# Optimization experiments

Measured on AMD Instinct MI355X. Metric: run time of the kernel, lower is better.

The kernel has to match this reference:

```python
import jax, jax.numpy as jnp
import numpy as np

B, N, D = 2, 4096, 1024
DS = 1024           # state_dim (defaults to embed_dim)
H = 4096            # mlp hidden = int(embed_dim * 4.0)
EPS = 1e-5


def _layernorm(x, w, b):
    mu = jnp.mean(x, axis=-1, keepdims=True)
    var = jnp.mean((x - mu) ** 2, axis=-1, keepdims=True)
    return (x - mu) * jax.lax.rsqrt(var + EPS) * w + b


def _selective_scan(deltaA, deltaB_u):
    # deltaA: (B, N, 1), deltaB_u: (B, N, DS). Recurrence h_i = dA_i * h + dBu_i.
    def step(h, inp):
        dA, dBu = inp           # (B,1), (B,DS)
        h = dA * h + dBu
        return h, h
    h0 = jnp.zeros((deltaB_u.shape[0], deltaB_u.shape[2]), deltaB_u.dtype)
    _, ys = jax.lax.scan(step, h0,
                         (jnp.swapaxes(deltaA, 0, 1), jnp.swapaxes(deltaB_u, 0, 1)))
    return jnp.swapaxes(ys, 0, 1)   # (B, N, DS)


def _forward(x, norm1_w, norm1_b, gate_w, gate_b, state_w, state_b,
             out_w, out_b, norm2_w, norm2_b, mlp_w1, mlp_b1, mlp_w2, mlp_b2):
    xn = _layernorm(x, norm1_w, norm1_b)
    g = xn @ gate_w + gate_b                       # (B,N,2D)
    gate, gate_gate = jnp.split(g, 2, axis=-1)
    gate = jax.nn.silu(gate)
    gate_gate = jax.nn.silu(gate_gate)
    u = (xn * gate) @ state_w + state_b            # (B,N,DS)
    Bm = gate_gate @ state_w + state_b             # (B,N,DS)
    # A = -ones(DS) -> delta*A = -delta broadcast over DS; keep (B,N,1)
    delta = jax.nn.softplus(jnp.mean(xn @ state_w + state_b, axis=-1, keepdims=True))
    deltaA = jnp.exp(-delta)                       # (B,N,1)
    deltaB_u = delta * Bm * u                      # (B,N,DS)
    # C = ones -> y_i = C_i * h_i = h_i
    y = _selective_scan(deltaA, deltaB_u)
    ssm_out = y @ out_w + out_b
    x = x + ssm_out
    x2 = _layernorm(x, norm2_w, norm2_b)
    mlp = jax.nn.gelu(x2 @ mlp_w1 + mlp_b1, approximate=False) @ mlp_w2 + mlp_b2
    return x + mlp


def setup_inputs() -> dict:
    key = jax.random.key(0)
    ks = jax.random.split(key, 12)
    s = 0.02
    p = lambda k, shape: jax.random.normal(k, shape, jnp.float32) * s
    return {
        "x": jax.random.normal(ks[0], (B, N, D), jnp.float32),
        "norm1_w": jnp.ones((D,), jnp.float32), "norm1_b": jnp.zeros((D,), jnp.float32),
        "gate_w": p(ks[1], (D, 2 * D)), "gate_b": p(ks[2], (2 * D,)),
        "state_w": p(ks[3], (D, DS)), "state_b": p(ks[4], (DS,)),
        "out_w": p(ks[5], (DS, D)), "out_b": p(ks[6], (D,)),
        "norm2_w": jnp.ones((D,), jnp.float32), "norm2_b": jnp.zeros((D,), jnp.float32),
        "mlp_w1": p(ks[7], (D, H)), "mlp_b1": p(ks[8], (H,)),
        "mlp_w2": p(ks[9], (H, D)), "mlp_b2": p(ks[10], (D,)),
    }


def reference(x, norm1_w, norm1_b, gate_w, gate_b, state_w, state_b,
              out_w, out_b, norm2_w, norm2_b, mlp_w1, mlp_b1, mlp_w2, mlp_b2):
    return _forward(x, norm1_w, norm1_b, gate_w, gate_b, state_w, state_b,
                    out_w, out_b, norm2_w, norm2_b, mlp_w1, mlp_b1, mlp_w2, mlp_b2)
```

## Files before the change

kernel.cpp:

```cpp
#include <hip/hip_runtime.h>
#include <hip/hip_bf16.h>
#include <math.h>

#define B_   2
#define N_   4096
#define D_   1024
#define DS_  1024
#define HID_ 4096
#define ROWS (B_ * N_)

#define CHK 128
#define TCH 32

typedef __attribute__((ext_vector_type(8))) short bf16x8;
typedef __attribute__((ext_vector_type(4))) float f32x4;

#define ASG __attribute__((address_space(1)))
#define AS3 __attribute__((address_space(3)))

__device__ __forceinline__ float bf2f(unsigned short u) {
  union { float f; unsigned int i; } v; v.i = ((unsigned int)u) << 16; return v.f;
}
__device__ __forceinline__ unsigned short f2bf(float f) {
  union { float f; unsigned int i; } v; v.f = f;
  unsigned int r = v.i + 0x7fffu + ((v.i >> 16) & 1u);
  return (unsigned short)(r >> 16);
}

__global__ void means_kernel(const float* __restrict__ W, const float* __restrict__ bvec,
                             float* __restrict__ swmean, float* __restrict__ sbmean) {
  __shared__ float sm[4];
  int bid = blockIdx.x, t = threadIdx.x;
  const float* src = (bid < D_) ? (W + (size_t)bid * DS_) : bvec;
  float s = 0.f;
  for (int j = t; j < DS_; j += 256) s += src[j];
  for (int o = 32; o; o >>= 1) s += __shfl_down(s, o);
  if ((t & 63) == 0) sm[t >> 6] = s;
  __syncthreads();
  if (t == 0) {
    float r = (sm[0] + sm[1] + sm[2] + sm[3]) * (1.f / DS_);
    if (bid < D_) swmean[bid] = r; else sbmean[0] = r;
  }
}

__global__ void transpose_all_kernel(const float* __restrict__ gw, const float* __restrict__ sw,
                                     const float* __restrict__ ow, const float* __restrict__ w1,
                                     const float* __restrict__ w2,
                                     unsigned short* __restrict__ gwT, unsigned short* __restrict__ swT,
                                     unsigned short* __restrict__ owT, unsigned short* __restrict__ w1T,
                                     unsigned short* __restrict__ w2T) {
  __shared__ float tile[32][33];
  int b = blockIdx.x;
  const float* W; unsigned short* WT; int K, N, t0;
  if (b < 2048)      { W = gw; WT = gwT; K = 1024; N = 2048; t0 = b; }
  else if (b < 3072) { W = sw; WT = swT; K = 1024; N = 1024; t0 = b - 2048; }
  else if (b < 4096) { W = ow; WT = owT; K = 1024; N = 1024; t0 = b - 3072; }
  else if (b < 8192) { W = w1; WT = w1T; K = 1024; N = 4096; t0 = b - 4096; }
  else               { W = w2; WT = w2T; K = 4096; N = 1024; t0 = b - 8192; }
  int ntx = N >> 5;
  int bn = (t0 % ntx) * 32, bk = (t0 / ntx) * 32;
  int tx = threadIdx.x & 31, ty = threadIdx.x >> 5;
  for (int i = ty; i < 32; i += 8)
    tile[i][tx] = W[(size_t)(bk + i) * N + bn + tx];
  __syncthreads();
  for (int i = ty; i < 32; i += 8)
    WT[(size_t)(bn + i) * K + bk + tx] = f2bf(tile[tx][i]);
}

template<bool WITH_DELTA>
__global__ void ln_kernel(const float* __restrict__ x, const float* __restrict__ w,
                          const float* __restrict__ bb, unsigned short* __restrict__ out_bf,
                          const float* __restrict__ swmean, const float* __restrict__ sbmean,
                          float* __restrict__ delta, float* __restrict__ ea) {
  __shared__ float sm[8];
  __shared__ float bc[2];
  int row = blockIdx.x, t = threadIdx.x;
  const float* xr = x + (size_t)row * D_;
  float4 xv = ((const float4*)xr)[t];
  float s  = xv.x + xv.y + xv.z + xv.w;
  float sq = xv.x * xv.x + xv.y * xv.y + xv.z * xv.z + xv.w * xv.w;
  for (int o = 32; o; o >>= 1) { s += __shfl_down(s, o); sq += __shfl_down(sq, o); }
  if ((t & 63) == 0) { sm[t >> 6] = s; sm[4 + (t >> 6)] = sq; }
  __syncthreads();
  if (t == 0) {
    float ts = sm[0] + sm[1] + sm[2] + sm[3];
    float tq = sm[4] + sm[5] + sm[6] + sm[7];
    float mu = ts * (1.f / D_);
    float var = tq * (1.f / D_) - mu * mu;
    bc[0] = mu; bc[1] = rsqrtf(var + 1e-5f);
  }
  __syncthreads();
  float mu = bc[0], rs = bc[1];
  float4 wv = ((const float4*)w)[t];
  float4 bv = ((const float4*)bb)[t];
  float n0 = (xv.x - mu) * rs * wv.x + bv.x;
  float n1 = (xv.y - mu) * rs * wv.y + bv.y;
  float n2 = (xv.z - mu) * rs * wv.z + bv.z;
  float n3 = (xv.w - mu) * rs * wv.w + bv.w;
  ushort4 o4; o4.x = f2bf(n0); o4.y = f2bf(n1); o4.z = f2bf(n2); o4.w = f2bf(n3);
  ((ushort4*)(out_bf + (size_t)row * D_))[t] = o4;
  if (WITH_DELTA) {
    float4 sw = ((const float4*)swmean)[t];
    float d = n0 * sw.x + n1 * sw.y + n2 * sw.z + n3 * sw.w;
    for (int o = 32; o; o >>= 1) d += __shfl_down(d, o);
    if ((t & 63) == 0) sm[t >> 6] = d;
    __syncthreads();
    if (t == 0) {
      float z = sm[0] + sm[1] + sm[2] + sm[3] + sbmean[0];
      float dl = (z > 15.f) ? z : log1pf(__expf(z));
      delta[row] = dl;
      ea[row] = __expf(-dl);
    }
  }
}


#define BARX { __builtin_amdgcn_s_barrier(); __builtin_amdgcn_sched_barrier(0); }

#define RD_A(TAU, H) { const char* ab_ = smem + ((((TAU)&1)*2+(H))<<14); \
  _Pragma("unroll") for (int mm_ = 0; mm_ < MB_H; ++mm_) \
  _Pragma("unroll") for (int ks_ = 0; ks_ < 2; ++ks_) { \
    int r_ = wr*(16*MB_H) + mm_*16 + l15; \
    int by_ = r_*128 + ks_*64 + kq16; by_ ^= ((by_>>7)&7)<<4; \
    af[mm_][ks_] = *(const bf16x8*)(ab_ + by_); } }

#define RD_B(TAU, H, DST) { const char* bb_ = smemB + ((((TAU)&1)*2+(H)))*SB; \
  _Pragma("unroll") for (int nn_ = 0; nn_ < NB_H; ++nn_) \
  _Pragma("unroll") for (int ks_ = 0; ks_ < 2; ++ks_) { \
    int r_ = wc*(16*NB_H) + nn_*16 + l15; \
    int by_ = r_*128 + ks_*64 + kq16; by_ ^= ((by_>>7)&7)<<4; \
    DST[nn_][ks_] = *(const bf16x8*)(bb_ + by_); } }

#define MFMAQ(QA, QB, BF) { __builtin_amdgcn_s_setprio(1); \
  _Pragma("unroll") for (int m_ = 0; m_ < MB_H; ++m_) \
  _Pragma("unroll") for (int n_ = 0; n_ < NB_H; ++n_) \
  _Pragma("unroll") for (int k_ = 0; k_ < 2; ++k_) \
    acc[(QA)*MB_H+m_][(QB)*NB_H+n_] = __builtin_amdgcn_mfma_f32_16x16x32_bf16( \
        af[m_][k_], BF[n_][k_], acc[(QA)*MB_H+m_][(QB)*NB_H+n_], 0, 0, 0); \
  __builtin_amdgcn_s_setprio(0); }

template<int BN, int EPI>
__global__ __launch_bounds__(512, 2) void gemm8p(
    const unsigned short* __restrict__ A1p, int lda1, int M1,
    const unsigned short* __restrict__ A2p, int lda2,
    const unsigned short* __restrict__ BT, const float* __restrict__ bias,
    void* __restrict__ Cout, const float* __restrict__ res,
    int N, int K, int nbx) {
  constexpr int WN   = (BN == 256) ? 4 : 2;
  constexpr int MB_H = (BN == 256) ? 4 : 2;
  constexpr int NB_H = 2;
  constexpr int MF   = 2 * MB_H;
  constexpr int LB   = BN / 128;
  constexpr int SB   = (BN / 2) * 64 * 2;
  __shared__ char smem[65536 + 4 * SB];
  char* smemB = smem + 65536;

  const int nwg = gridDim.x;
  int bid = blockIdx.x;
  int wg = (bid & 7) * (nwg >> 3) + (bid >> 3);
  const int bx = wg % nbx, by = wg / nbx;
  const int mbase = by * 256, nbase = bx * BN;

  const int tid = threadIdx.x;
  const int lane = tid & 63, wid = tid >> 6;
  const int wr = wid / WN, wc = wid % WN;
  const int l15 = lane & 15, kq16 = (lane >> 4) * 16;
  const int wvoff16 = wid << 10;

  const unsigned short* Ause; int ldaU;
  if (mbase < M1) { Ause = A1p + (size_t)mbase * lda1; ldaU = lda1; }
  else            { Ause = A2p + (size_t)(mbase - M1) * lda2; ldaU = lda2; }

  int L0 = tid * 16;        int b0 = L0 ^ (((L0 >> 7) & 7) << 4);
  int L1 = 8192 + tid * 16; int b1 = L1 ^ (((L1 >> 7) & 7) << 4);
  const unsigned short* pA0 = Ause + (size_t)(b0 >> 7) * ldaU + ((b0 & 127) >> 1);
  const unsigned short* pA1 = Ause + (size_t)(b1 >> 7) * ldaU + ((b1 & 127) >> 1);
  const unsigned short* pB0 = BT + (size_t)(nbase + (b0 >> 7)) * K + ((b0 & 127) >> 1);
  const unsigned short* pB1 = BT + (size_t)(nbase + (b1 >> 7)) * K + ((b1 & 127) >> 1);

  auto stageA = [&](int tau, int h, bool en) {
    if (!en) return;
    char* l0 = smem + (((tau & 1) * 2 + h) << 14) + wvoff16;
    const unsigned short* g0 = pA0 + (size_t)h * 128 * ldaU + tau * 64;
    const unsigned short* g1 = pA1 + (size_t)h * 128 * ldaU + tau * 64;
    __builtin_amdgcn_global_load_lds((const ASG void*)g0, (AS3 void*)l0, 16, 0, 0);
    __builtin_amdgcn_global_load_lds((const ASG void*)g1, (AS3 void*)(l0 + 8192), 16, 0, 0);
  };
  auto stageB = [&](int tau, int h, bool en) {
    if (!en) return;
    char* l0 = smemB + ((tau & 1) * 2 + h) * SB + wvoff16;
    const unsigned short* g0 = pB0 + (size_t)h * (BN / 2) * K + tau * 64;
    __builtin_amdgcn_global_load_lds((const ASG void*)g0, (AS3 void*)l0, 16, 0, 0);
    if constexpr (LB == 2) {
      const unsigned short* g1 = pB1 + (size_t)h * (BN / 2) * K + tau * 64;
      __builtin_amdgcn_global_load_lds((const ASG void*)g1, (AS3 void*)(l0 + 8192), 16, 0, 0);
    }
  };
  auto vm_steady = [&]() {
    if constexpr (BN == 256) { asm volatile("s_waitcnt vmcnt(6)" ::: "memory"); }
    else                     { asm volatile("s_waitcnt vmcnt(5)" ::: "memory"); }
  };

  f32x4 acc[MF][4];
#pragma unroll
  for (int m = 0; m < MF; ++m)
#pragma unroll
    for (int n = 0; n < 4; ++n) acc[m][n] = (f32x4){0.f, 0.f, 0.f, 0.f};
  bf16x8 af[MB_H][2], bq0[NB_H][2], bq1[NB_H][2];

  const int NT = K >> 6, NI = NT >> 1;

  stageA(0, 0, true); stageB(0, 0, true); stageA(0, 1, true); stageB(0, 1, true);
  stageA(1, 0, true); stageB(1, 0, true); stageA(1, 1, true);
  vm_steady();
  BARX;

#pragma unroll 1
  for (int i = 0; i < NI; ++i) {
    const int t0 = 2 * i;
    const bool st = (i < NI - 1);
    stageB(t0 + 1, 1, true); RD_A(t0, 0); RD_B(t0, 0, bq0);
    BARX; MFMAQ(0, 0, bq0); BARX;
    stageA(t0 + 2, 0, st); RD_B(t0, 1, bq1);
    BARX; MFMAQ(0, 1, bq1); BARX;
    stageB(t0 + 2, 0, st); RD_A(t0, 1);
    BARX; MFMAQ(1, 1, bq1); BARX;
    stageA(t0 + 2, 1, st);
    if (st) { vm_steady(); } else { asm volatile("s_waitcnt vmcnt(0)" ::: "memory"); }
    BARX; MFMAQ(1, 0, bq0); BARX;
    stageB(t0 + 2, 1, st); RD_A(t0 + 1, 0); RD_B(t0 + 1, 0, bq0);
    BARX; MFMAQ(0, 0, bq0); BARX;
    stageA(t0 + 3, 0, st); RD_B(t0 + 1, 1, bq1);
    BARX; MFMAQ(0, 1, bq1); BARX;
    stageB(t0 + 3, 0, st); RD_A(t0 + 1, 1);
    BARX; MFMAQ(1, 1, bq1); BARX;
    stageA(t0 + 3, 1, st);
    if (st) vm_steady();
    BARX; MFMAQ(1, 0, bq0); BARX;
  }

  const int r0 = (lane >> 4) * 4;
#pragma unroll
  for (int mb = 0; mb < MF; ++mb) {
    int row = mbase + wr * (16 * MB_H) + (mb % MB_H) * 16 + (mb / MB_H) * 128 + r0;
#pragma unroll
    for (int nb = 0; nb < 4; ++nb) {
      int col = nbase + wc * (16 * NB_H) + (nb % NB_H) * 16 + (nb / NB_H) * (BN / 2) + l15;
      float bc = bias[col];
#pragma unroll
      for (int r = 0; r < 4; ++r) {
        float v = acc[mb][nb][r] + bc;
        size_t off = (size_t)(row + r) * N + col;
        if (EPI == 1) {
          v = v / (1.f + __expf(-v));
          ((unsigned short*)Cout)[off] = f2bf(v);
        } else if (EPI == 2) {
          ((unsigned short*)Cout)[off] = f2bf(v);
        } else if (EPI == 3) {
          ((float*)Cout)[off] = v + res[off];
        } else if (EPI == 4) {
          float tt = v * (0.7978845608f + 0.0356774081f * v * v);
          v = v / (1.f + __expf(-2.f * tt));
          ((unsigned short*)Cout)[off] = f2bf(v);
        }
      }
    }
  }
}

__global__ void ew_xg_kernel(const unsigned short* __restrict__ xn,
                             const unsigned short* __restrict__ gs,
                             unsigned short* __restrict__ xg) {
  size_t i8 = ((size_t)blockIdx.x * 256 + threadIdx.x) * 8;
  size_t row = i8 >> 10, col = i8 & 1023;
  uint4 xv = *(const uint4*)(xn + i8);
  uint4 gv = *(const uint4*)(gs + row * 2048 + col);
  const unsigned short* xs = (const unsigned short*)&xv;
  const unsigned short* gg = (const unsigned short*)&gv;
  uint4 ov; unsigned short* o = (unsigned short*)&ov;
#pragma unroll
  for (int j = 0; j < 8; ++j) o[j] = f2bf(bf2f(xs[j]) * bf2f(gg[j]));
  *(uint4*)(xg + i8) = ov;
}

__global__ void scan_a_kernel(const unsigned short* __restrict__ u,
                              const unsigned short* __restrict__ bm,
                              const float* __restrict__ delta,
                              const float* __restrict__ ea,
                              float* __restrict__ hend, float* __restrict__ P) {
  int blk = blockIdx.x;
  int b = blk / CHK, c = blk % CHK;
  int ch = threadIdx.x;
  size_t base = ((size_t)(b * N_ + c * TCH)) * DS_ + ch;
  const float* dp = delta + b * N_ + c * TCH;
  const float* ep = ea + b * N_ + c * TCH;
  float h = 0.f, pa = 1.f;
#pragma unroll 4
  for (int t = 0; t < TCH; ++t) {
    float dl = dp[t], e = ep[t];
    float du = dl * bf2f(u[base + (size_t)t * DS_]) * bf2f(bm[base + (size_t)t * DS_]);
    h = e * h + du;
    pa *= e;
  }
  hend[(size_t)blk * DS_ + ch] = h;
  if (ch == 0) P[blk] = pa;
}

__global__ void scan_combine_kernel(const float* __restrict__ hend, const float* __restrict__ P,
                                    float* __restrict__ carryin) {
  int b = blockIdx.x, ch = threadIdx.x;
  float carry = 0.f;
  for (int c = 0; c < CHK; ++c) {
    size_t o = (size_t)(b * CHK + c) * DS_ + ch;
    carryin[o] = carry;
    carry = P[b * CHK + c] * carry + hend[o];
  }
}

__global__ void scan_b_kernel(const unsigned short* __restrict__ u,
                              const unsigned short* __restrict__ bm,
                              const float* __restrict__ delta,
                              const float* __restrict__ ea,
                              const float* __restrict__ carryin,
                              unsigned short* __restrict__ y) {
  int blk = blockIdx.x;
  int b = blk / CHK, c = blk % CHK;
  int ch = threadIdx.x;
  size_t base = ((size_t)(b * N_ + c * TCH)) * DS_ + ch;
  const float* dp = delta + b * N_ + c * TCH;
  const float* ep = ea + b * N_ + c * TCH;
  float h = carryin[(size_t)blk * DS_ + ch];
#pragma unroll 4
  for (int t = 0; t < TCH; ++t) {
    float dl = dp[t], e = ep[t];
    float du = dl * bf2f(u[base + (size_t)t * DS_]) * bf2f(bm[base + (size_t)t * DS_]);
    h = e * h + du;
    y[base + (size_t)t * DS_] = f2bf(h);
  }
}

extern "C" void kernel_launch(void* const* d_in, const int* in_sizes, int n_in,
                              void* d_out, int out_size, void* d_ws, size_t ws_size,
                              hipStream_t stream) {
  const float* x       = (const float*)d_in[0];
  const float* n1w     = (const float*)d_in[1];
  const float* n1b     = (const float*)d_in[2];
  const float* gate_w  = (const float*)d_in[3];
  const float* gate_b  = (const float*)d_in[4];
  const float* state_w = (const float*)d_in[5];
  const float* state_b = (const float*)d_in[6];
  const float* out_w   = (const float*)d_in[7];
  const float* out_b   = (const float*)d_in[8];
  const float* n2w     = (const float*)d_in[9];
  const float* n2b     = (const float*)d_in[10];
  const float* mlp_w1  = (const float*)d_in[11];
  const float* mlp_b1  = (const float*)d_in[12];
  const float* mlp_w2  = (const float*)d_in[13];
  const float* mlp_b2  = (const float*)d_in[14];
  float* outp = (float*)d_out;

  char* w = (char*)d_ws;
  size_t off = 0;
  auto alloc = [&](size_t bytes) { char* p = w + off; off += (bytes + 255) & ~(size_t)255; return p; };

  unsigned short* gate_wT  = (unsigned short*)alloc((size_t)2048 * 1024 * 2);
  unsigned short* state_wT = (unsigned short*)alloc((size_t)1024 * 1024 * 2);
  unsigned short* out_wT   = (unsigned short*)alloc((size_t)1024 * 1024 * 2);
  unsigned short* w1T      = (unsigned short*)alloc((size_t)4096 * 1024 * 2);
  unsigned short* w2T      = (unsigned short*)alloc((size_t)1024 * 4096 * 2);
  float* swmean  = (float*)alloc(D_ * 4);
  float* sbmean  = (float*)alloc(256);
  float* delta   = (float*)alloc((size_t)ROWS * 4);
  float* eadel   = (float*)alloc((size_t)ROWS * 4);
  float* hend    = (float*)alloc((size_t)B_ * CHK * DS_ * 4);
  float* carryin = (float*)alloc((size_t)B_ * CHK * DS_ * 4);
  float* P       = (float*)alloc((size_t)B_ * CHK * 4);
  unsigned short* xn = (unsigned short*)alloc((size_t)ROWS * D_ * 2);
  unsigned short* gs = (unsigned short*)alloc((size_t)ROWS * HID_ * 2);
  unsigned short* xg = (unsigned short*)alloc((size_t)ROWS * D_ * 2);
  float* x1          = (float*)alloc((size_t)ROWS * D_ * 4);

  unsigned short* h1 = gs;
  unsigned short* y  = xg;
  unsigned short* x2 = xg;
  unsigned short* u  = (unsigned short*)x1;
  unsigned short* bm = u + (size_t)ROWS * D_;

  means_kernel<<<D_ + 1, 256, 0, stream>>>(state_w, state_b, swmean, sbmean);
  transpose_all_kernel<<<12288, 256, 0, stream>>>(gate_w, state_w, out_w, mlp_w1, mlp_w2,
                                                  gate_wT, state_wT, out_wT, w1T, w2T);

  ln_kernel<true><<<ROWS, 256, 0, stream>>>(x, n1w, n1b, xn, swmean, sbmean, delta, eadel);

  const int BIG = 1 << 30;
  gemm8p<256, 1><<<256, 512, 0, stream>>>(xn, 1024, BIG, xn, 1024,
                                          gate_wT, gate_b, gs, nullptr, 2048, 1024, 8);
  ew_xg_kernel<<<(ROWS * D_) / 8 / 256, 256, 0, stream>>>(xn, gs, xg);
  gemm8p<256, 2><<<256, 512, 0, stream>>>(xg, 1024, 8192, gs + 1024, 2048,
                                          state_wT, state_b, u, nullptr, 1024, 1024, 4);

  scan_a_kernel<<<B_ * CHK, 1024, 0, stream>>>(u, bm, delta, eadel, hend, P);
  scan_combine_kernel<<<B_, 1024, 0, stream>>>(hend, P, carryin);
  scan_b_kernel<<<B_ * CHK, 1024, 0, stream>>>(u, bm, delta, eadel, carryin, y);

  gemm8p<128, 3><<<256, 512, 0, stream>>>(y, 1024, BIG, y, 1024,
                                          out_wT, out_b, x1, x, 1024, 1024, 8);
  ln_kernel<false><<<ROWS, 256, 0, stream>>>(x1, n2w, n2b, x2, nullptr, nullptr, nullptr, nullptr);
  gemm8p<256, 4><<<512, 512, 0, stream>>>(x2, 1024, BIG, x2, 1024,
                                          w1T, mlp_b1, h1, nullptr, 4096, 1024, 16);
  gemm8p<128, 3><<<256, 512, 0, stream>>>(h1, 4096, BIG, h1, 4096,
                                          w2T, mlp_b2, outp, x1, 1024, 4096, 8);
}
```

Before: 355.8 us.

## Store residual x1 in bf16 and use K32-step GEMM variant for MLP up-projection

The out-projection epilogue now writes the residual sum x1 as bf16 rather than fp32. The second layernorm and the final MLP-down epilogue read that bf16 tensor, which halves traffic on the intermediate. A new gemm8p32 kernel with a 32-wide K step, smaller shared memory and launch bounds of 4 blocks per SM replaces gemm8p<256> for the MLP up-projection, aiming for higher occupancy. Rounding the residual stream to bf16 loses precision that is added back into the output.

```diff
diff --git a/kernel.cpp b/kernel.cpp
--- a/kernel.cpp
+++ b/kernel.cpp
@@ -67,18 +67,26 @@
     WT[(size_t)(bn + i) * K + bk + tx] = f2bf(tile[tx][i]);
 }
 
-template<bool WITH_DELTA>
-__global__ void ln_kernel(const float* __restrict__ x, const float* __restrict__ w,
+template<bool WITH_DELTA, bool BF16IN>
+__global__ void ln_kernel(const void* __restrict__ xin, const float* __restrict__ w,
                           const float* __restrict__ bb, unsigned short* __restrict__ out_bf,
                           const float* __restrict__ swmean, const float* __restrict__ sbmean,
                           float* __restrict__ delta, float* __restrict__ ea) {
   __shared__ float sm[8];
   __shared__ float bc[2];
   int row = blockIdx.x, t = threadIdx.x;
-  const float* xr = x + (size_t)row * D_;
-  float4 xv = ((const float4*)xr)[t];
-  float s  = xv.x + xv.y + xv.z + xv.w;
-  float sq = xv.x * xv.x + xv.y * xv.y + xv.z * xv.z + xv.w * xv.w;
+  float x0, x1, x2, x3;
+  if (BF16IN) {
+    const unsigned short* xr = (const unsigned short*)xin + (size_t)row * D_;
+    ushort4 xv = ((const ushort4*)xr)[t];
+    x0 = bf2f(xv.x); x1 = bf2f(xv.y); x2 = bf2f(xv.z); x3 = bf2f(xv.w);
+  } else {
+    const float* xr = (const float*)xin + (size_t)row * D_;
+    float4 xv = ((const float4*)xr)[t];
+    x0 = xv.x; x1 = xv.y; x2 = xv.z; x3 = xv.w;
+  }
+  float s  = x0 + x1 + x2 + x3;
+  float sq = x0 * x0 + x1 * x1 + x2 * x2 + x3 * x3;
   for (int o = 32; o; o >>= 1) { s += __shfl_down(s, o); sq += __shfl_down(sq, o); }
   if ((t & 63) == 0) { sm[t >> 6] = s; sm[4 + (t >> 6)] = sq; }
   __syncthreads();
@@ -93,10 +101,10 @@
   float mu = bc[0], rs = bc[1];
   float4 wv = ((const float4*)w)[t];
   float4 bv = ((const float4*)bb)[t];
-  float n0 = (xv.x - mu) * rs * wv.x + bv.x;
-  float n1 = (xv.y - mu) * rs * wv.y + bv.y;
-  float n2 = (xv.z - mu) * rs * wv.z + bv.z;
-  float n3 = (xv.w - mu) * rs * wv.w + bv.w;
+  float n0 = (x0 - mu) * rs * wv.x + bv.x;
+  float n1 = (x1 - mu) * rs * wv.y + bv.y;
+  float n2 = (x2 - mu) * rs * wv.z + bv.z;
+  float n3 = (x3 - mu) * rs * wv.w + bv.w;
   ushort4 o4; o4.x = f2bf(n0); o4.y = f2bf(n1); o4.z = f2bf(n2); o4.w = f2bf(n3);
   ((ushort4*)(out_bf + (size_t)row * D_))[t] = o4;
   if (WITH_DELTA) {
@@ -138,6 +146,26 @@
     acc[(QA)*MB_H+m_][(QB)*NB_H+n_] = __builtin_amdgcn_mfma_f32_16x16x32_bf16( \
         af[m_][k_], BF[n_][k_], acc[(QA)*MB_H+m_][(QB)*NB_H+n_], 0, 0, 0); \
   __builtin_amdgcn_s_setprio(0); }
+
+template<int EPI>
+__device__ __forceinline__ void epi_store(float v, size_t off, void* Cout, const float* res) {
+  if (EPI == 1) {
+    v = v / (1.f + __expf(-v));
+    ((unsigned short*)Cout)[off] = f2bf(v);
+  } else if (EPI == 2) {
+    ((unsigned short*)Cout)[off] = f2bf(v);
+  } else if (EPI == 3) {
+    ((float*)Cout)[off] = v + res[off];
+  } else if (EPI == 4) {
+    float tt = v * (0.7978845608f + 0.0356774081f * v * v);
+    v = v / (1.f + __expf(-2.f * tt));
+    ((unsigned short*)Cout)[off] = f2bf(v);
+  } else if (EPI == 6) {
+    ((unsigned short*)Cout)[off] = f2bf(v + res[off]);
+  } else if (EPI == 7) {
+    ((float*)Cout)[off] = v + bf2f(((const unsigned short*)res)[off]);
+  }
+}
 
 template<int BN, int EPI>
 __global__ __launch_bounds__(512, 2) void gemm8p(
@@ -248,22 +276,118 @@
       int col = nbase + wc * (16 * NB_H) + (nb % NB_H) * 16 + (nb / NB_H) * (BN / 2) + l15;
       float bc = bias[col];
 #pragma unroll
-      for (int r = 0; r < 4; ++r) {
-        float v = acc[mb][nb][r] + bc;
-        size_t off = (size_t)(row + r) * N + col;
-        if (EPI == 1) {
-          v = v / (1.f + __expf(-v));
-          ((unsigned short*)Cout)[off] = f2bf(v);
-        } else if (EPI == 2) {
-          ((unsigned short*)Cout)[off] = f2bf(v);
-        } else if (EPI == 3) {
-          ((float*)Cout)[off] = v + res[off];
-        } else if (EPI == 4) {
-          float tt = v * (0.7978845608f + 0.0356774081f * v * v);
-          v = v / (1.f + __expf(-2.f * tt));
-          ((unsigned short*)Cout)[off] = f2bf(v);
-        }
-      }
+      for (int r = 0; r < 4; ++r)
+        epi_store<EPI>(acc[mb][nb][r] + bc, (size_t)(row + r) * N + col, Cout, res);
+    }
+  }
+}
+
+
+#define RD_A32(TAU, H) { const char* ab_ = smem + ((((TAU)&1)*2+(H))<<13); \
+  _Pragma("unroll") for (int mm_ = 0; mm_ < 4; ++mm_) { \
+    int r_ = wr*64 + mm_*16 + l15; \
+    int by_ = r_*64 + kq16; by_ ^= ((by_>>7)&3)<<4; \
+    af[mm_] = *(const bf16x8*)(ab_ + by_); } }
+
+#define RD_B32(TAU, H, DST) { const char* bb_ = smemB + ((((TAU)&1)*2+(H))<<13); \
+  _Pragma("unroll") for (int nn_ = 0; nn_ < 2; ++nn_) { \
+    int r_ = wc*32 + nn_*16 + l15; \
+    int by_ = r_*64 + kq16; by_ ^= ((by_>>7)&3)<<4; \
+    DST[nn_] = *(const bf16x8*)(bb_ + by_); } }
+
+#define MFMAQ32(QA, QB, BF) { __builtin_amdgcn_s_setprio(1); \
+  _Pragma("unroll") for (int m_ = 0; m_ < 4; ++m_) \
+  _Pragma("unroll") for (int n_ = 0; n_ < 2; ++n_) \
+    acc[(QA)*4+m_][(QB)*2+n_] = __builtin_amdgcn_mfma_f32_16x16x32_bf16( \
+        af[m_], BF[n_], acc[(QA)*4+m_][(QB)*2+n_], 0, 0, 0); \
+  __builtin_amdgcn_s_setprio(0); }
+
+template<int EPI>
+__global__ __launch_bounds__(512, 4) void gemm8p32(
+    const unsigned short* __restrict__ A1p, int lda1,
+    const unsigned short* __restrict__ BT, const float* __restrict__ bias,
+    void* __restrict__ Cout, const float* __restrict__ res,
+    int N, int K, int nbx) {
+  __shared__ char smem[65536];
+  char* smemB = smem + 32768;
+  const int nwg = gridDim.x;
+  int bid = blockIdx.x;
+  int wg = (bid & 7) * (nwg >> 3) + (bid >> 3);
+  const int bx = wg % nbx, by = wg / nbx;
+  const int mbase = by * 256, nbase = bx * 256;
+  const int tid = threadIdx.x;
+  const int lane = tid & 63, wid = tid >> 6;
+  const int wr = wid >> 2, wc = wid & 3;
+  const int l15 = lane & 15, kq16 = (lane >> 4) * 16;
+
+  const unsigned short* Ause = A1p + (size_t)mbase * lda1;
+  int L0 = tid * 16; int b0 = L0 ^ (((L0 >> 7) & 3) << 4);
+  const unsigned short* pA0 = Ause + (size_t)(b0 >> 6) * lda1 + ((b0 & 63) >> 1);
+  const unsigned short* pB0 = BT + (size_t)(nbase + (b0 >> 6)) * K + ((b0 & 63) >> 1);
+
+  auto stageA = [&](int tau, int h, bool en) {
+    if (!en) return;
+    char* l0 = smem + (((tau & 1) * 2 + h) << 13) + tid * 16;
+    const unsigned short* g0 = pA0 + (size_t)h * 128 * lda1 + tau * 32;
+    __builtin_amdgcn_global_load_lds((const ASG void*)g0, (AS3 void*)l0, 16, 0, 0);
+  };
+  auto stageB = [&](int tau, int h, bool en) {
+    if (!en) return;
+    char* l0 = smemB + (((tau & 1) * 2 + h) << 13) + tid * 16;
+    const unsigned short* g0 = pB0 + (size_t)h * 128 * K + tau * 32;
+    __builtin_amdgcn_global_load_lds((const ASG void*)g0, (AS3 void*)l0, 16, 0, 0);
+  };
+
+  f32x4 acc[8][4];
+#pragma unroll
+  for (int m = 0; m < 8; ++m)
+#pragma unroll
+    for (int n = 0; n < 4; ++n) acc[m][n] = (f32x4){0.f, 0.f, 0.f, 0.f};
+  bf16x8 af[4], bq0[2], bq1[2];
+
+  const int NT = K >> 5, NI = NT >> 1;
+
+  stageA(0, 0, true); stageB(0, 0, true); stageA(0, 1, true); stageB(0, 1, true);
+  stageA(1, 0, true); stageB(1, 0, true); stageA(1, 1, true);
+  asm volatile("s_waitcnt vmcnt(3)" ::: "memory");
+  BARX;
+
+#pragma unroll 1
+  for (int i = 0; i < NI; ++i) {
+    const int t0 = 2 * i;
+    const bool st = (i < NI - 1);
+    stageB(t0 + 1, 1, true); RD_A32(t0, 0); RD_B32(t0, 0, bq0);
+    BARX; MFMAQ32(0, 0, bq0); BARX;
+    stageA(t0 + 2, 0, st); RD_B32(t0, 1, bq1);
+    BARX; MFMAQ32(0, 1, bq1); BARX;
+    stageB(t0 + 2, 0, st); RD_A32(t0, 1);
+    BARX; MFMAQ32(1, 1, bq1); BARX;
+    stageA(t0 + 2, 1, st);
+    if (st) { asm volatile("s_waitcnt vmcnt(3)" ::: "memory"); }
+    else    { asm volatile("s_waitcnt vmcnt(0)" ::: "memory"); }
+    BARX; MFMAQ32(1, 0, bq0); BARX;
+    stageB(t0 + 2, 1, st); RD_A32(t0 + 1, 0); RD_B32(t0 + 1, 0, bq0);
+    BARX; MFMAQ32(0, 0, bq0); BARX;
+    stageA(t0 + 3, 0, st); RD_B32(t0 + 1, 1, bq1);
+    BARX; MFMAQ32(0, 1, bq1); BARX;
+    stageB(t0 + 3, 0, st); RD_A32(t0 + 1, 1);
+    BARX; MFMAQ32(1, 1, bq1); BARX;
+    stageA(t0 + 3, 1, st);
+    if (st) { asm volatile("s_waitcnt vmcnt(3)" ::: "memory"); }
+    BARX; MFMAQ32(1, 0, bq0); BARX;
+  }
+
+  const int r0 = (lane >> 4) * 4;
+#pragma unroll
+  for (int mb = 0; mb < 8; ++mb) {
+    int row = mbase + wr * 64 + (mb % 4) * 16 + (mb / 4) * 128 + r0;
+#pragma unroll
+    for (int nb = 0; nb < 4; ++nb) {
+      int col = nbase + wc * 32 + (nb % 2) * 16 + (nb / 2) * 128 + l15;
+      float bc = bias[col];
+#pragma unroll
+      for (int r = 0; r < 4; ++r)
+        epi_store<EPI>(acc[mb][nb][r] + bc, (size_t)(row + r) * N + col, Cout, res);
     }
   }
 }
@@ -378,19 +502,20 @@
   unsigned short* xn = (unsigned short*)alloc((size_t)ROWS * D_ * 2);
   unsigned short* gs = (unsigned short*)alloc((size_t)ROWS * HID_ * 2);
   unsigned short* xg = (unsigned short*)alloc((size_t)ROWS * D_ * 2);
-  float* x1          = (float*)alloc((size_t)ROWS * D_ * 4);
-
-  unsigned short* h1 = gs;
-  unsigned short* y  = xg;
-  unsigned short* x2 = xg;
-  unsigned short* u  = (unsigned short*)x1;
-  unsigned short* bm = u + (size_t)ROWS * D_;
+  float* x1f         = (float*)alloc((size_t)ROWS * D_ * 4);
+
+  unsigned short* h1  = gs;
+  unsigned short* y   = xg;
+  unsigned short* x2  = xg;
+  unsigned short* u   = (unsigned short*)x1f;
+  unsigned short* bm  = u + (size_t)ROWS * D_;
+  unsigned short* x1b = u;
 
   means_kernel<<<D_ + 1, 256, 0, stream>>>(state_w, state_b, swmean, sbmean);
   transpose_all_kernel<<<12288, 256, 0, stream>>>(gate_w, state_w, out_w, mlp_w1, mlp_w2,
                                                   gate_wT, state_wT, out_wT, w1T, w2T);
 
-  ln_kernel<true><<<ROWS, 256, 0, stream>>>(x, n1w, n1b, xn, swmean, sbmean, delta, eadel);
+  ln_kernel<true, false><<<ROWS, 256, 0, stream>>>(x, n1w, n1b, xn, swmean, sbmean, delta, eadel);
 
   const int BIG = 1 << 30;
   gemm8p<256, 1><<<256, 512, 0, stream>>>(xn, 1024, BIG, xn, 1024,
@@ -403,11 +528,10 @@
   scan_combine_kernel<<<B_, 1024, 0, stream>>>(hend, P, carryin);
   scan_b_kernel<<<B_ * CHK, 1024, 0, stream>>>(u, bm, delta, eadel, carryin, y);
 
-  gemm8p<128, 3><<<256, 512, 0, stream>>>(y, 1024, BIG, y, 1024,
-                                          out_wT, out_b, x1, x, 1024, 1024, 8);
-  ln_kernel<false><<<ROWS, 256, 0, stream>>>(x1, n2w, n2b, x2, nullptr, nullptr, nullptr, nullptr);
-  gemm8p<256, 4><<<512, 512, 0, stream>>>(x2, 1024, BIG, x2, 1024,
-                                          w1T, mlp_b1, h1, nullptr, 4096, 1024, 16);
-  gemm8p<128, 3><<<256, 512, 0, stream>>>(h1, 4096, BIG, h1, 4096,
-                                          w2T, mlp_b2, outp, x1, 1024, 4096, 8);
-}
+  gemm8p<128, 6><<<256, 512, 0, stream>>>(y, 1024, BIG, y, 1024,
+                                          out_wT, out_b, x1b, x, 1024, 1024, 8);
+  ln_kernel<false, true><<<ROWS, 256, 0, stream>>>(x1b, n2w, n2b, x2, nullptr, nullptr, nullptr, nullptr);
+  gemm8p32<4><<<512, 512, 0, stream>>>(x2, 1024, w1T, mlp_b1, h1, nullptr, 4096, 1024, 16);
+  gemm8p<128, 7><<<256, 512, 0, stream>>>(h1, 4096, BIG, h1, 4096,
+                                          w2T, mlp_b2, outp, (const float*)x1b, 1024, 4096, 8);
+}
```

Measured after the change: 936.1 us. +163.1%, slower.
